# Performance work log

Measured on AMD Instinct MI355X. Metric: run time of the kernel, lower is better.

## Reference

```python
import jax, jax.numpy as jnp
import numpy as np

D = 512          # d_model
S = D // 2       # d_state
NL = 6           # num_layers
EVERY = 4        # attention_every
WIN = 256        # window_size
H = 8            # num_heads
DH = D // H      # head_dim
EPS = 1e-5


def layer_norm(x, gamma, beta):
    mu = jnp.mean(x, axis=-1, keepdims=True)
    var = jnp.mean((x - mu) ** 2, axis=-1, keepdims=True)
    return (x - mu) * jax.lax.rsqrt(var + EPS) * gamma + beta


def mamba_layer(seq, state, conv_w, Wx, Wh, Wout, A):
    """Lightweight Mamba-style update returning a (B, D) state summary.

    causal depthwise conv (k=3) -> SiLU -> project to d_state -> diagonal
    linear SSM scan (computed in closed form since the decay is constant)
    -> read out final state back to d_model.
    """
    B, L, _ = seq.shape
    xp = jnp.pad(seq, ((0, 0), (2, 0), (0, 0)))  # causal pad, kernel 3
    x = conv_w[0] * xp[:, :L] + conv_w[1] * xp[:, 1:L + 1] + conv_w[2] * xp[:, 2:L + 2]
    x = jax.nn.silu(x)
    u = jnp.einsum('bld,ds->bls', x, Wx)          # (B, L, S)
    a = jax.nn.sigmoid(A)                          # (S,) decay in (0,1)
    powers = (L - 1) - jnp.arange(L, dtype=jnp.float32)  # (L,)
    w = a[None, :] ** powers[:, None]              # (L, S)
    h0 = state @ Wh                                # (B, S)
    hT = (a ** L) * h0 + jnp.einsum('bls,ls->bs', u, w)
    return hT @ Wout                               # (B, D)


def local_attention(seq, Wqkv, bqkv, Wo, bo):
    B, L, _ = seq.shape
    qkv = seq @ Wqkv.T + bqkv                      # (B, L, 3D)
    q, k, v = jnp.split(qkv, 3, axis=-1)
    q = q.reshape(B, L, H, DH).transpose(0, 2, 1, 3)
    k = k.reshape(B, L, H, DH).transpose(0, 2, 1, 3)
    v = v.reshape(B, L, H, DH).transpose(0, 2, 1, 3)
    idx = jnp.arange(L)
    band = jnp.abs(idx[:, None] - idx[None, :]) <= WIN
    mask = jnp.where(band, 0.0, -jnp.inf).astype(seq.dtype)  # (L, L)
    scores = jnp.einsum('bhqd,bhkd->bhqk', q, k) / np.sqrt(DH) + mask
    attn = jax.nn.softmax(scores, axis=-1)
    out = jnp.einsum('bhqk,bhkd->bhqd', attn, v)
    out = out.transpose(0, 2, 1, 3).reshape(B, L, D)
    return out @ Wo.T + bo


def setup_inputs() -> dict:
    key = jax.random.key(0)
    ks = jax.random.split(key, 12)
    B, L = 4, 2048
    sc = 0.02
    return {
        'context': jax.random.normal(ks[0], (B, L, D), jnp.float32),
        'conv_w': jax.random.normal(ks[1], (NL, 3, D), jnp.float32) * sc,
        'Wx': jax.random.normal(ks[2], (NL, D, S), jnp.float32) * sc,
        'Wh': jax.random.normal(ks[3], (NL, D, S), jnp.float32) * sc,
        'Wout': jax.random.normal(ks[4], (NL, S, D), jnp.float32) * sc,
        'A': jax.random.normal(ks[5], (NL, S), jnp.float32),
        'gamma_m': jnp.ones((D,), jnp.float32),
        'beta_m': jnp.zeros((D,), jnp.float32),
        'gamma_a': jnp.ones((D,), jnp.float32),
        'beta_a': jnp.zeros((D,), jnp.float32),
        'Wqkv': jax.random.normal(ks[6], (3 * D, D), jnp.float32) * sc,
        'bqkv': jnp.zeros((3 * D,), jnp.float32),
        'Wo': jax.random.normal(ks[7], (D, D), jnp.float32) * sc,
        'bo': jnp.zeros((D,), jnp.float32),
    }


def reference(context, conv_w, Wx, Wh, Wout, A, gamma_m, beta_m, gamma_a, beta_a, Wqkv, bqkv, Wo, bo):
    B = context.shape[0]
    seq = context
    state = jnp.zeros((B, D), context.dtype)  # initial_state=None
    for i in range(NL):
        state = mamba_layer(seq, state, conv_w[i], Wx[i], Wh[i], Wout[i], A[i])
        seq = layer_norm(seq + state[:, None, :], gamma_m, beta_m)
        if (i + 1) % EVERY == 0:
            attn_out = local_attention(seq, Wqkv, bqkv, Wo, bo)
            seq = layer_norm(seq + attn_out, gamma_a, beta_a)
    return seq
```

## Files before the change

### kernel.cpp

```cpp
#include <hip/hip_runtime.h>

#define B_ 4
#define L_ 2048
#define D_ 512
#define S_ 256
#define H_ 8
#define DH_ 64
#define WIN_ 256
#define EPS_ 1e-5f
#define LOG2E_ 1.4426950408889634f
#define UWIN_ 768
#define UCHUNKS_ 6

using f32x4 = __attribute__((ext_vector_type(4))) float;
using s16x8 = __attribute__((ext_vector_type(8))) short;

__device__ __forceinline__ unsigned short f2b(float f) {
  unsigned int u = __builtin_bit_cast(unsigned int, f);
  u += 0x7FFFu + ((u >> 16) & 1u);
  return (unsigned short)(u >> 16);
}
__device__ __forceinline__ float b2f(unsigned short u) {
  return __builtin_bit_cast(float, (unsigned int)u << 16);
}

__device__ __forceinline__ float silu(float y) { return y / (1.f + expf(-y)); }

__device__ __forceinline__ void gll16(const void* g, void* l) {
  __builtin_amdgcn_global_load_lds((const __attribute__((address_space(1))) void*)g,
                                   (__attribute__((address_space(3))) void*)l, 16, 0, 0);
}

__global__ __launch_bounds__(256) void k_f2b(const float* __restrict__ in,
                                             unsigned short* __restrict__ out, int n4) {
  int i = blockIdx.x * 256 + threadIdx.x;
  if (i >= n4) return;
  float4 v = reinterpret_cast<const float4*>(in)[i];
  ushort4 o;
  o.x = f2b(v.x); o.y = f2b(v.y); o.z = f2b(v.z); o.w = f2b(v.w);
  reinterpret_cast<ushort4*>(out)[i] = o;
}

__global__ void k_twx(const float* __restrict__ wx, unsigned short* __restrict__ wxt) {
  __shared__ float tile[32][33];
  int lyr = blockIdx.z;
  int d0 = blockIdx.x * 32, s0 = blockIdx.y * 32;
  const float* src = wx + (size_t)lyr * D_ * S_;
  unsigned short* dst = wxt + (size_t)lyr * S_ * D_;
  for (int r = threadIdx.y; r < 32; r += 8)
    tile[r][threadIdx.x] = src[(size_t)(d0 + r) * S_ + s0 + threadIdx.x];
  __syncthreads();
  for (int r = threadIdx.y; r < 32; r += 8)
    dst[(size_t)(s0 + r) * D_ + d0 + threadIdx.x] = f2b(tile[threadIdx.x][r]);
}

__global__ __launch_bounds__(128) void k_conv_silu(const float* __restrict__ seq,
                                                   const float* __restrict__ cw,
                                                   unsigned short* __restrict__ x) {
  int bl = blockIdx.x;
  int l = bl & (L_ - 1);
  int t = threadIdx.x;
  const float4* s4 = reinterpret_cast<const float4*>(seq);
  const float4* c4 = reinterpret_cast<const float4*>(cw);
  size_t row = (size_t)bl * 128;
  float4 c0 = c4[t], c1 = c4[128 + t], c2 = c4[256 + t];
  float4 z = make_float4(0.f, 0.f, 0.f, 0.f);
  float4 s0 = (l >= 2) ? s4[row - 256 + t] : z;
  float4 s1 = (l >= 1) ? s4[row - 128 + t] : z;
  float4 s2 = s4[row + t];
  float y0 = c0.x * s0.x + c1.x * s1.x + c2.x * s2.x;
  float y1 = c0.y * s0.y + c1.y * s1.y + c2.y * s2.y;
  float y2 = c0.z * s0.z + c1.z * s1.z + c2.z * s2.z;
  float y3 = c0.w * s0.w + c1.w * s1.w + c2.w * s2.w;
  ushort4 o;
  o.x = f2b(silu(y0)); o.y = f2b(silu(y1)); o.z = f2b(silu(y2)); o.w = f2b(silu(y3));
  reinterpret_cast<ushort4*>(x)[row + t] = o;
}

__global__ __launch_bounds__(64) void k_lnconv(const void* __restrict__ seqIn, int in_bf16,
                                               const float* __restrict__ add, int addfull,
                                               const float* __restrict__ gamma,
                                               const float* __restrict__ beta,
                                               unsigned short* __restrict__ outBf,
                                               float* __restrict__ outF32,
                                               unsigned short* __restrict__ xbf,
                                               const float* __restrict__ cw) {
  int t = threadIdx.x;
  int r0 = blockIdx.x * 8;
  int b = r0 >> 11, l0 = r0 & (L_ - 1);
  bool hasconv = (cw != nullptr);
  const float4* in4 = reinterpret_cast<const float4*>(seqIn);
  const s16x8* inb = reinterpret_cast<const s16x8*>(seqIn);
  const float4* ad4 = reinterpret_cast<const float4*>(add);
  float4 g0 = reinterpret_cast<const float4*>(gamma)[2 * t];
  float4 g1 = reinterpret_cast<const float4*>(gamma)[2 * t + 1];
  float4 be0 = reinterpret_cast<const float4*>(beta)[2 * t];
  float4 be1 = reinterpret_cast<const float4*>(beta)[2 * t + 1];
  float4 av0, av1;
  if (!addfull) { av0 = ad4[b * 128 + 2 * t]; av1 = ad4[b * 128 + 2 * t + 1]; }
  float4 c0a, c0b, c1a, c1b, c2a, c2b;
  if (hasconv) {
    const float4* c4 = reinterpret_cast<const float4*>(cw);
    c0a = c4[2 * t]; c0b = c4[2 * t + 1];
    c1a = c4[128 + 2 * t]; c1b = c4[128 + 2 * t + 1];
    c2a = c4[256 + 2 * t]; c2b = c4[256 + 2 * t + 1];
  }
  float4 z = make_float4(0.f, 0.f, 0.f, 0.f);
  float4 m2a = z, m2b = z, m1a = z, m1b = z;
  int nrows = hasconv ? 10 : 8;
  int lstart = hasconv ? l0 - 2 : l0;
  for (int j = 0; j < nrows; ++j) {
    int l = lstart + j;
    float4 oa = z, ob = z;
    if (l >= 0) {
      size_t r4 = ((size_t)(b * L_ + l)) * 128;
      float4 v0, v1;
      if (in_bf16) {
        s16x8 v8 = inb[((size_t)(b * L_ + l)) * 64 + t];
        v0.x = b2f((unsigned short)v8[0]); v0.y = b2f((unsigned short)v8[1]);
        v0.z = b2f((unsigned short)v8[2]); v0.w = b2f((unsigned short)v8[3]);
        v1.x = b2f((unsigned short)v8[4]); v1.y = b2f((unsigned short)v8[5]);
        v1.z = b2f((unsigned short)v8[6]); v1.w = b2f((unsigned short)v8[7]);
      } else {
        v0 = in4[r4 + 2 * t]; v1 = in4[r4 + 2 * t + 1];
      }
      float4 a0, a1;
      if (addfull) { a0 = ad4[r4 + 2 * t]; a1 = ad4[r4 + 2 * t + 1]; }
      else { a0 = av0; a1 = av1; }
      v0.x += a0.x; v0.y += a0.y; v0.z += a0.z; v0.w += a0.w;
      v1.x += a1.x; v1.y += a1.y; v1.z += a1.z; v1.w += a1.w;
      float sx = v0.x + v0.y + v0.z + v0.w + v1.x + v1.y + v1.z + v1.w;
      float sq = v0.x * v0.x + v0.y * v0.y + v0.z * v0.z + v0.w * v0.w +
                 v1.x * v1.x + v1.y * v1.y + v1.z * v1.z + v1.w * v1.w;
#pragma unroll
      for (int off = 1; off < 64; off <<= 1) {
        sx += __shfl_xor(sx, off);
        sq += __shfl_xor(sq, off);
      }
      float mu = sx * (1.f / D_);
      float var = sq * (1.f / D_) - mu * mu;
      float rstd = rsqrtf(var + EPS_);
      oa.x = (v0.x - mu) * rstd * g0.x + be0.x;
      oa.y = (v0.y - mu) * rstd * g0.y + be0.y;
      oa.z = (v0.z - mu) * rstd * g0.z + be0.z;
      oa.w = (v0.w - mu) * rstd * g0.w + be0.w;
      ob.x = (v1.x - mu) * rstd * g1.x + be1.x;
      ob.y = (v1.y - mu) * rstd * g1.y + be1.y;
      ob.z = (v1.z - mu) * rstd * g1.z + be1.z;
      ob.w = (v1.w - mu) * rstd * g1.w + be1.w;
      if (l >= l0) {
        if (outBf) {
          s16x8 sb;
          sb[0] = (short)f2b(oa.x); sb[1] = (short)f2b(oa.y);
          sb[2] = (short)f2b(oa.z); sb[3] = (short)f2b(oa.w);
          sb[4] = (short)f2b(ob.x); sb[5] = (short)f2b(ob.y);
          sb[6] = (short)f2b(ob.z); sb[7] = (short)f2b(ob.w);
          *reinterpret_cast<s16x8*>(outBf + ((size_t)(b * L_ + l)) * 512 + t * 8) = sb;
        }
        if (outF32) {
          float4* o4 = reinterpret_cast<float4*>(outF32);
          o4[r4 + 2 * t] = oa;
          o4[r4 + 2 * t + 1] = ob;
        }
      }
    }
    if (hasconv && j >= 2) {
      float y0 = c0a.x * m2a.x + c1a.x * m1a.x + c2a.x * oa.x;
      float y1 = c0a.y * m2a.y + c1a.y * m1a.y + c2a.y * oa.y;
      float y2 = c0a.z * m2a.z + c1a.z * m1a.z + c2a.z * oa.z;
      float y3 = c0a.w * m2a.w + c1a.w * m1a.w + c2a.w * oa.w;
      float y4 = c0b.x * m2b.x + c1b.x * m1b.x + c2b.x * ob.x;
      float y5 = c0b.y * m2b.y + c1b.y * m1b.y + c2b.y * ob.y;
      float y6 = c0b.z * m2b.z + c1b.z * m1b.z + c2b.z * ob.z;
      float y7 = c0b.w * m2b.w + c1b.w * m1b.w + c2b.w * ob.w;
      s16x8 xo;
      xo[0] = (short)f2b(silu(y0)); xo[1] = (short)f2b(silu(y1));
      xo[2] = (short)f2b(silu(y2)); xo[3] = (short)f2b(silu(y3));
      xo[4] = (short)f2b(silu(y4)); xo[5] = (short)f2b(silu(y5));
      xo[6] = (short)f2b(silu(y6)); xo[7] = (short)f2b(silu(y7));
      *reinterpret_cast<s16x8*>(xbf + ((size_t)(b * L_ + l)) * 512 + t * 8) = xo;
    }
    m2a = m1a; m2b = m1b; m1a = oa; m1b = ob;
  }
}

__device__ __forceinline__ void g128_core(const unsigned short* __restrict__ A,
                                          const unsigned short* __restrict__ Bt,
                                          int K, int m0, int n0, int k_lo, int k_hi,
                                          unsigned short* As, unsigned short* Bs,
                                          f32x4 (&acc)[4][4]) {
  int t = threadIdx.x;
  int lane = t & 63;
  int g = lane >> 4, mr = lane & 15;
  int wid = t >> 6, wr = wid >> 1, wc = wid & 1;
#pragma unroll
  for (int i = 0; i < 4; ++i)
#pragma unroll
    for (int j = 0; j < 4; ++j) { f32x4 z = {0.f, 0.f, 0.f, 0.f}; acc[i][j] = z; }
  int r0 = t >> 2, p = (t & 3) * 8;
  const unsigned short* ag0 = A + (size_t)(m0 + r0) * K + p;
  const unsigned short* ag1 = ag0 + (size_t)64 * K;
  const unsigned short* bg0 = Bt + (size_t)(n0 + r0) * K + p;
  const unsigned short* bg1 = bg0 + (size_t)64 * K;
  int woff = wid * 512;
  gll16(ag0 + k_lo, As + woff);
  gll16(ag1 + k_lo, As + 2048 + woff);
  gll16(bg0 + k_lo, Bs + woff);
  gll16(bg1 + k_lo, Bs + 2048 + woff);
  int nsteps = (k_hi - k_lo) >> 5;
  int cur = 0;
  for (int s = 0; s < nsteps; ++s) {
    int k0 = k_lo + (s << 5);
    if (s + 1 < nsteps) {
      int nb = (cur ^ 1) * 4096;
      gll16(ag0 + k0 + 32, As + nb + woff);
      gll16(ag1 + k0 + 32, As + nb + 2048 + woff);
      gll16(bg0 + k0 + 32, Bs + nb + woff);
      gll16(bg1 + k0 + 32, Bs + nb + 2048 + woff);
      asm volatile("s_waitcnt vmcnt(4)" ::: "memory");
    } else {
      asm volatile("s_waitcnt vmcnt(0)" ::: "memory");
    }
    __builtin_amdgcn_sched_barrier(0);
    __builtin_amdgcn_s_barrier();
    __builtin_amdgcn_sched_barrier(0);
    const unsigned short* Ar = As + cur * 4096;
    const unsigned short* Br = Bs + cur * 4096;
    s16x8 af[4], bf[4];
#pragma unroll
    for (int fm = 0; fm < 4; ++fm)
      af[fm] = *reinterpret_cast<const s16x8*>(Ar + (size_t)(wr * 64 + fm * 16 + mr) * 32 + g * 8);
#pragma unroll
    for (int fn = 0; fn < 4; ++fn)
      bf[fn] = *reinterpret_cast<const s16x8*>(Br + (size_t)(wc * 64 + fn * 16 + mr) * 32 + g * 8);
#pragma unroll
    for (int fm = 0; fm < 4; ++fm)
#pragma unroll
      for (int fn = 0; fn < 4; ++fn)
        acc[fm][fn] = __builtin_amdgcn_mfma_f32_16x16x32_bf16(af[fm], bf[fn], acc[fm][fn], 0, 0, 0);
    __builtin_amdgcn_sched_barrier(0);
    __builtin_amdgcn_s_barrier();
    cur ^= 1;
  }
}

__device__ __forceinline__ int xcd_lb(int bid, int nwg) {
  return (bid & 7) * (nwg >> 3) + (bid >> 3);
}

__global__ __launch_bounds__(256) void k_g128(const unsigned short* __restrict__ A,
                                              const unsigned short* __restrict__ Bt,
                                              float* __restrict__ C,
                                              const float* __restrict__ bias,
                                              int N, int K, int ntn) {
  __shared__ __align__(16) unsigned short As[8192], Bs[8192];
  int lb = xcd_lb(blockIdx.x, gridDim.x);
  int m0 = (lb / ntn) * 128, n0 = (lb % ntn) * 128;
  f32x4 acc[4][4];
  g128_core(A, Bt, K, m0, n0, 0, K, As, Bs, acc);
  int t = threadIdx.x, lane = t & 63, g = lane >> 4, mr = lane & 15;
  int wid = t >> 6, wr = wid >> 1, wc = wid & 1;
#pragma unroll
  for (int fm = 0; fm < 4; ++fm)
#pragma unroll
    for (int fn = 0; fn < 4; ++fn) {
      int row = m0 + wr * 64 + fm * 16 + g * 4;
      int col = n0 + wc * 64 + fn * 16 + mr;
      float badd = bias ? bias[col] : 0.f;
#pragma unroll
      for (int q = 0; q < 4; ++q)
        C[(size_t)(row + q) * N + col] = acc[fm][fn][q] + badd;
    }
}

__global__ __launch_bounds__(256) void k_g128_qkv(const unsigned short* __restrict__ A,
                                                  const unsigned short* __restrict__ Bt,
                                                  const float* __restrict__ bias,
                                                  unsigned short* __restrict__ Qbf,
                                                  unsigned short* __restrict__ Kbf,
                                                  unsigned short* __restrict__ VbfT) {
  __shared__ __align__(16) unsigned short sm[16384];
  int lb = xcd_lb(blockIdx.x, gridDim.x);
  int m0 = (lb / 12) * 128, n0 = (lb % 12) * 128;
  f32x4 acc[4][4];
  g128_core(A, Bt, 512, m0, n0, 0, 512, sm, sm + 8192, acc);
  int t = threadIdx.x, lane = t & 63, g = lane >> 4, mr = lane & 15;
  int wid = t >> 6, wr = wid >> 1, wc = wid & 1;
  int b = m0 >> 11, l0 = m0 & (L_ - 1);
  if (n0 < 1024) {
#pragma unroll
    for (int fm = 0; fm < 4; ++fm)
#pragma unroll
      for (int fn = 0; fn < 4; ++fn) {
        int row0 = m0 + wr * 64 + fm * 16 + g * 4;
        int col = n0 + wc * 64 + fn * 16 + mr;
        int sec = col >> 9;
        int hh = (col >> 6) & 7;
        int dh = col & 63;
        float badd = bias[col];
        float scale = (sec == 0) ? 0.125f : 1.f;
        unsigned short* dstbase = (sec == 0) ? Qbf : Kbf;
#pragma unroll
        for (int q = 0; q < 4; ++q) {
          int row = row0 + q;
          int bb = row >> 11, l = row & (L_ - 1);
          dstbase[(((size_t)(bb * H_ + hh)) * L_ + l) * 64 + dh] =
              f2b((acc[fm][fn][q] + badd) * scale);
        }
      }
  } else {
#pragma unroll
    for (int chalf = 0; chalf < 2; ++chalf) {
      __syncthreads();
      if (wc == chalf) {
#pragma unroll
        for (int fm = 0; fm < 4; ++fm)
#pragma unroll
          for (int fn = 0; fn < 4; ++fn) {
            int col = n0 + wc * 64 + fn * 16 + mr;
            float badd = bias[col];
            int col_local = fn * 16 + mr;
            int row_local = wr * 64 + fm * 16 + g * 4;
            ushort4 pk;
            pk.x = f2b(acc[fm][fn][0] + badd);
            pk.y = f2b(acc[fm][fn][1] + badd);
            pk.z = f2b(acc[fm][fn][2] + badd);
            pk.w = f2b(acc[fm][fn][3] + badd);
            *reinterpret_cast<ushort4*>(&sm[col_local * 136 + row_local]) = pk;
          }
      }
      __syncthreads();
      int c = t >> 2, lp = (t & 3) * 32;
      int h = ((n0 - 1024) >> 6) + chalf;
      unsigned short* dst = VbfT + (((size_t)(b * H_ + h)) * 64 + c) * L_ + l0 + lp;
#pragma unroll
      for (int u = 0; u < 4; ++u)
        *reinterpret_cast<s16x8*>(dst + u * 8) =
            *reinterpret_cast<const s16x8*>(&sm[c * 136 + lp + u * 8]);
    }
  }
}

__global__ __launch_bounds__(256) void k_g128_u(const unsigned short* __restrict__ A,
                                                const unsigned short* __restrict__ Bt,
                                                const float* __restrict__ Ap,
                                                float* __restrict__ part3) {
  __shared__ __align__(16) unsigned short As[8192], Bs[8192];
  int lb = xcd_lb(blockIdx.x, gridDim.x);
  int mt = lb >> 3;
  int rr = lb & 7;
  int nt = rr >> 2, kz = rr & 3;
  int b = mt / UCHUNKS_, cc = mt % UCHUNKS_;
  int m0 = b * L_ + (L_ - UWIN_) + cc * 128;
  int n0 = nt * 128;
  f32x4 acc[4][4];
  g128_core(A, Bt, 512, m0, n0, kz * 128, kz * 128 + 128, As, Bs, acc);
  int t = threadIdx.x, lane = t & 63, g = lane >> 4, mr = lane & 15;
  int wid = t >> 6, wr = wid >> 1, wc = wid & 1;
  float wsum[4];
#pragma unroll
  for (int fn = 0; fn < 4; ++fn) {
    int col = n0 + wc * 64 + fn * 16 + mr;
    float a = 1.f / (1.f + expf(-Ap[col]));
    float la2 = log2f(a);
    float s = 0.f;
#pragma unroll
    for (int fm = 0; fm < 4; ++fm) {
      int rbase = (m0 + wr * 64 + fm * 16 + g * 4) & (L_ - 1);
#pragma unroll
      for (int q = 0; q < 4; ++q) {
        float e = (float)(2047 - (rbase + q));
        s += acc[fm][fn][q] * exp2f(e * la2);
      }
    }
    s += __shfl_xor(s, 16);
    s += __shfl_xor(s, 32);
    wsum[fn] = s;
  }
  float* red = (float*)As;
  __syncthreads();
  if (wr == 0 && g == 0) {
#pragma unroll
    for (int fn = 0; fn < 4; ++fn) red[(wc * 4 + fn) * 16 + mr] = wsum[fn];
  }
  __syncthreads();
  if (wr == 1 && g == 0) {
#pragma unroll
    for (int fn = 0; fn < 4; ++fn) {
      int col = n0 + wc * 64 + fn * 16 + mr;
      part3[(((size_t)(b * UCHUNKS_ + cc)) * 4 + kz) * 256 + col] =
          wsum[fn] + red[(wc * 4 + fn) * 16 + mr];
    }
  }
}

__global__ __launch_bounds__(256) void k_tail(const float* __restrict__ part3,
                                              const float* __restrict__ Wout,
                                              float* __restrict__ state) {
  int bz = blockIdx.x;
  int b = bz >> 4, dl = (bz & 15) * 32;
  int t = threadIdx.x;
  __shared__ float hTs[256];
  __shared__ float red[8][33];
  float acc = 0.f;
#pragma unroll
  for (int c = 0; c < UCHUNKS_ * 4; ++c)
    acc += part3[((size_t)b * UCHUNKS_ * 4 + c) * 256 + t];
  hTs[t] = acc;
  __syncthreads();
  int dx = t & 31, sy = t >> 5;
  float p = 0.f;
  for (int j = 0; j < 32; ++j) {
    int s = sy * 32 + j;
    p += hTs[s] * Wout[(size_t)s * 512 + dl + dx];
  }
  red[sy][dx] = p;
  __syncthreads();
  if (t < 32) {
    float a = 0.f;
#pragma unroll
    for (int k = 0; k < 8; ++k) a += red[k][t];
    state[b * 512 + dl + t] = a;
  }
}

__global__ __launch_bounds__(256) void k_fattn(const unsigned short* __restrict__ Qbf,
                                               const unsigned short* __restrict__ Kbf,
                                               const unsigned short* __restrict__ VbfT,
                                               unsigned short* __restrict__ attnbf) {
  __shared__ __align__(16) unsigned short Ks[64][72];
  __shared__ __align__(16) unsigned short Vt[64][72];
  __shared__ __align__(16) unsigned short Ps[4][16][72];
  int b = blockIdx.z, h = blockIdx.y, q0 = blockIdx.x * 64;
  int t = threadIdx.x;
  int lane = t & 63, wid = t >> 6;
  int g = lane >> 4, mr = lane & 15;
  const unsigned short* Qp = Qbf + ((size_t)(b * H_ + h)) * L_ * 64;
  const unsigned short* Kp = Kbf + ((size_t)(b * H_ + h)) * L_ * 64;
  const unsigned short* VpT = VbfT + ((size_t)(b * H_ + h)) * 64 * L_;
  int qbase = q0 + wid * 16;
  s16x8 qf0 = *reinterpret_cast<const s16x8*>(Qp + (size_t)(qbase + mr) * 64 + g * 8);
  s16x8 qf1 = *reinterpret_cast<const s16x8*>(Qp + (size_t)(qbase + mr) * 64 + 32 + g * 8);
  f32x4 oacc[4];
#pragma unroll
  for (int fn = 0; fn < 4; ++fn) { f32x4 zz = {0.f, 0.f, 0.f, 0.f}; oacc[fn] = zz; }
  float lsum[4] = {0.f, 0.f, 0.f, 0.f};
  int kstart = q0 - WIN_; if (kstart < 0) kstart = 0;
  int kend = q0 + 64 + WIN_; if (kend > L_) kend = L_;

  for (int kt = kstart; kt < kend; kt += 64) {
    __syncthreads();
#pragma unroll
    for (int it = 0; it < 2; ++it) {
      int chunk = t + it * 256;
      int row = chunk >> 3, c8 = (chunk & 7) * 8;
      *reinterpret_cast<s16x8*>(&Ks[row][c8]) =
          *reinterpret_cast<const s16x8*>(Kp + (size_t)(kt + row) * 64 + c8);
      *reinterpret_cast<s16x8*>(&Vt[row][c8]) =
          *reinterpret_cast<const s16x8*>(VpT + (size_t)row * L_ + kt + c8);
    }
    __syncthreads();
    f32x4 sacc[4];
#pragma unroll
    for (int n = 0; n < 4; ++n) {
      f32x4 zz = {0.f, 0.f, 0.f, 0.f};
      sacc[n] = zz;
      s16x8 kf0 = *reinterpret_cast<const s16x8*>(&Ks[n * 16 + mr][g * 8]);
      s16x8 kf1 = *reinterpret_cast<const s16x8*>(&Ks[n * 16 + mr][32 + g * 8]);
      sacc[n] = __builtin_amdgcn_mfma_f32_16x16x32_bf16(qf0, kf0, sacc[n], 0, 0, 0);
      sacc[n] = __builtin_amdgcn_mfma_f32_16x16x32_bf16(qf1, kf1, sacc[n], 0, 0, 0);
    }
    bool needmask = (kt - q0 > 192) || (q0 - kt > 192);
#pragma unroll
    for (int reg = 0; reg < 4; ++reg) {
      int q_abs = qbase + g * 4 + reg;
#pragma unroll
      for (int n = 0; n < 4; ++n) {
        float pv = exp2f(sacc[n][reg] * LOG2E_);
        if (needmask) {
          int key = kt + n * 16 + mr;
          int dd = key - q_abs; dd = dd < 0 ? -dd : dd;
          if (dd > WIN_) pv = 0.f;
        }
        lsum[reg] += pv;
        Ps[wid][g * 4 + reg][n * 16 + mr] = f2b(pv);
      }
    }
    s16x8 pa0 = *reinterpret_cast<const s16x8*>(&Ps[wid][mr][g * 8]);
    s16x8 pa1 = *reinterpret_cast<const s16x8*>(&Ps[wid][mr][32 + g * 8]);
#pragma unroll
    for (int fn = 0; fn < 4; ++fn) {
      s16x8 vf0 = *reinterpret_cast<const s16x8*>(&Vt[fn * 16 + mr][g * 8]);
      s16x8 vf1 = *reinterpret_cast<const s16x8*>(&Vt[fn * 16 + mr][32 + g * 8]);
      oacc[fn] = __builtin_amdgcn_mfma_f32_16x16x32_bf16(pa0, vf0, oacc[fn], 0, 0, 0);
      oacc[fn] = __builtin_amdgcn_mfma_f32_16x16x32_bf16(pa1, vf1, oacc[fn], 0, 0, 0);
    }
  }
#pragma unroll
  for (int reg = 0; reg < 4; ++reg) {
    float ls = lsum[reg];
#pragma unroll
    for (int off = 1; off < 16; off <<= 1) ls += __shfl_xor(ls, off);
    float inv = 1.f / ls;
    int q_abs = qbase + g * 4 + reg;
    unsigned short* dst = attnbf + ((size_t)(b * L_ + q_abs)) * 512 + h * 64;
#pragma unroll
    for (int fn = 0; fn < 4; ++fn)
      dst[fn * 16 + mr] = f2b(oacc[fn][reg] * inv);
  }
}

extern "C" void kernel_launch(void* const* d_in, const int* in_sizes, int n_in,
                              void* d_out, int out_size, void* d_ws, size_t ws_size,
                              hipStream_t stream) {
  const float* context = (const float*)d_in[0];
  const float* conv_w  = (const float*)d_in[1];
  const float* Wx      = (const float*)d_in[2];
  const float* Wout    = (const float*)d_in[4];
  const float* Aparm   = (const float*)d_in[5];
  const float* gamma_m = (const float*)d_in[6];
  const float* beta_m  = (const float*)d_in[7];
  const float* gamma_a = (const float*)d_in[8];
  const float* beta_a  = (const float*)d_in[9];
  const float* Wqkv    = (const float*)d_in[10];
  const float* bqkv    = (const float*)d_in[11];
  const float* Wo      = (const float*)d_in[12];
  const float* bo      = (const float*)d_in[13];
  float* outF = (float*)d_out;
  float* ws = (float*)d_ws;

  float* proj = ws;
  unsigned short* Qbf    = (unsigned short*)(ws);
  unsigned short* Kbf    = (unsigned short*)(ws + 2097152);
  unsigned short* seqAb  = (unsigned short*)(ws + 4194304);
  unsigned short* seqBb  = (unsigned short*)(ws + 6291456);
  unsigned short* VbfT   = (unsigned short*)(ws + 8388608);
  unsigned short* xbf    = (unsigned short*)(ws + 10485760);
  unsigned short* attnbf = (unsigned short*)(ws + 12582912);
  unsigned short* wqkvbf = (unsigned short*)(ws + 14680064);
  unsigned short* wobf   = (unsigned short*)(ws + 15073280);
  unsigned short* wxtbf  = (unsigned short*)(ws + 15204352);
  float* state = ws + 15597568;
  float* part3 = state + 2048;

  k_f2b<<<768, 256, 0, stream>>>(Wqkv, wqkvbf, 196608);
  k_f2b<<<256, 256, 0, stream>>>(Wo, wobf, 65536);
  k_twx<<<dim3(16, 8, 6), dim3(32, 8), 0, stream>>>(Wx, wxtbf);

  k_conv_silu<<<B_ * L_, 128, 0, stream>>>(context, conv_w, xbf);

  for (int i = 0; i < 6; ++i) {
    k_g128_u<<<B_ * UCHUNKS_ * 8, 256, 0, stream>>>(
        xbf, wxtbf + (size_t)i * S_ * D_, Aparm + (size_t)i * S_, part3);
    k_tail<<<64, 256, 0, stream>>>(part3, Wout + (size_t)i * S_ * D_, state);
    const float* cwn = conv_w + (size_t)(i + 1) * 3 * D_;
    switch (i) {
      case 0:
        k_lnconv<<<1024, 64, 0, stream>>>(context, 0, state, 0, gamma_m, beta_m,
                                          seqAb, nullptr, xbf, cwn);
        break;
      case 1:
        k_lnconv<<<1024, 64, 0, stream>>>(seqAb, 1, state, 0, gamma_m, beta_m,
                                          seqBb, nullptr, xbf, cwn);
        break;
      case 2:
        k_lnconv<<<1024, 64, 0, stream>>>(seqBb, 1, state, 0, gamma_m, beta_m,
                                          seqAb, nullptr, xbf, cwn);
        break;
      case 3:
        k_lnconv<<<1024, 64, 0, stream>>>(seqAb, 1, state, 0, gamma_m, beta_m,
                                          seqAb, nullptr, nullptr, nullptr);
        k_g128_qkv<<<768, 256, 0, stream>>>(seqAb, wqkvbf, bqkv, Qbf, Kbf, VbfT);
        k_fattn<<<dim3(32, 8, 4), 256, 0, stream>>>(Qbf, Kbf, VbfT, attnbf);
        k_g128<<<256, 256, 0, stream>>>(attnbf, wobf, proj, bo, 512, 512, 4);
        k_lnconv<<<1024, 64, 0, stream>>>(seqAb, 1, proj, 1, gamma_a, beta_a,
                                          seqBb, nullptr, xbf, cwn);
        break;
      case 4:
        k_lnconv<<<1024, 64, 0, stream>>>(seqBb, 1, state, 0, gamma_m, beta_m,
                                          seqAb, nullptr, xbf, cwn);
        break;
      case 5:
        k_lnconv<<<1024, 64, 0, stream>>>(seqAb, 1, state, 0, gamma_m, beta_m,
                                          nullptr, outF, nullptr, nullptr);
        break;
    }
  }
}
```

Baseline: 257.8 us.

## Fuse SSM tail into u-GEMM via last-block atomic counter; merge weight casts

Removes the separate k_tail launch per layer. The last GEMM block to finish for each batch, found through an atomic counter, now reduces the partial sums and does the Wout readout itself. The two fp32-to-bf16 weight conversion kernels are merged into one launch. The cost is that the readout now runs on only 4 blocks, one per batch, each doing a serial 256-step loop instead of spreading over 64 blocks. It also adds a memset and threadfence overhead.

After: 395.6 us. 53.4% more time.

```diff
diff --git a/kernel.cpp b/kernel.cpp
--- a/kernel.cpp
+++ b/kernel.cpp
@@ -31,14 +31,20 @@
                                    (__attribute__((address_space(3))) void*)l, 16, 0, 0);
 }
 
-__global__ __launch_bounds__(256) void k_f2b(const float* __restrict__ in,
-                                             unsigned short* __restrict__ out, int n4) {
+__global__ __launch_bounds__(256) void k_f2b2(const float* __restrict__ inA,
+                                              unsigned short* __restrict__ outA, int na4,
+                                              const float* __restrict__ inB,
+                                              unsigned short* __restrict__ outB, int nb4) {
   int i = blockIdx.x * 256 + threadIdx.x;
-  if (i >= n4) return;
-  float4 v = reinterpret_cast<const float4*>(in)[i];
+  const float* src;
+  unsigned short* dst;
+  int j;
+  if (i < na4) { src = inA; dst = outA; j = i; }
+  else { j = i - na4; if (j >= nb4) return; src = inB; dst = outB; }
+  float4 v = reinterpret_cast<const float4*>(src)[j];
   ushort4 o;
   o.x = f2b(v.x); o.y = f2b(v.y); o.z = f2b(v.z); o.w = f2b(v.w);
-  reinterpret_cast<ushort4*>(out)[i] = o;
+  reinterpret_cast<ushort4*>(dst)[j] = o;
 }
 
 __global__ void k_twx(const float* __restrict__ wx, unsigned short* __restrict__ wxt) {
@@ -341,11 +347,15 @@
   }
 }
 
-__global__ __launch_bounds__(256) void k_g128_u(const unsigned short* __restrict__ A,
-                                                const unsigned short* __restrict__ Bt,
-                                                const float* __restrict__ Ap,
-                                                float* __restrict__ part3) {
+__global__ __launch_bounds__(256) void k_g128_ut(const unsigned short* __restrict__ A,
+                                                 const unsigned short* __restrict__ Bt,
+                                                 const float* __restrict__ Ap,
+                                                 float* __restrict__ part3,
+                                                 const float* __restrict__ Wout,
+                                                 float* __restrict__ state,
+                                                 int* __restrict__ cnt) {
   __shared__ __align__(16) unsigned short As[8192], Bs[8192];
+  __shared__ int isLast;
   int lb = xcd_lb(blockIdx.x, gridDim.x);
   int mt = lb >> 3;
   int rr = lb & 7;
@@ -392,35 +402,31 @@
           wsum[fn] + red[(wc * 4 + fn) * 16 + mr];
     }
   }
-}
-
-__global__ __launch_bounds__(256) void k_tail(const float* __restrict__ part3,
-                                              const float* __restrict__ Wout,
-                                              float* __restrict__ state) {
-  int bz = blockIdx.x;
-  int b = bz >> 4, dl = (bz & 15) * 32;
-  int t = threadIdx.x;
-  __shared__ float hTs[256];
-  __shared__ float red[8][33];
-  float acc = 0.f;
-#pragma unroll
-  for (int c = 0; c < UCHUNKS_ * 4; ++c)
-    acc += part3[((size_t)b * UCHUNKS_ * 4 + c) * 256 + t];
-  hTs[t] = acc;
+  __threadfence();
   __syncthreads();
-  int dx = t & 31, sy = t >> 5;
-  float p = 0.f;
-  for (int j = 0; j < 32; ++j) {
-    int s = sy * 32 + j;
-    p += hTs[s] * Wout[(size_t)s * 512 + dl + dx];
-  }
-  red[sy][dx] = p;
+  if (t == 0) {
+    int v = atomicAdd(&cnt[b], 1);
+    isLast = (v == 47) ? 1 : 0;
+  }
   __syncthreads();
-  if (t < 32) {
-    float a = 0.f;
-#pragma unroll
-    for (int k = 0; k < 8; ++k) a += red[k][t];
-    state[b * 512 + dl + t] = a;
+  if (isLast) {
+    __threadfence();
+    float h = 0.f;
+#pragma unroll
+    for (int c = 0; c < UCHUNKS_ * 4; ++c)
+      h += __hip_atomic_load(&part3[((size_t)b * UCHUNKS_ * 4 + c) * 256 + t],
+                             __ATOMIC_RELAXED, __HIP_MEMORY_SCOPE_AGENT);
+    float* hTs = (float*)As;
+    hTs[t] = h;
+    __syncthreads();
+    float s0 = 0.f, s1 = 0.f;
+    for (int s = 0; s < 256; ++s) {
+      float hv = hTs[s];
+      s0 += hv * Wout[(size_t)s * 512 + t];
+      s1 += hv * Wout[(size_t)s * 512 + t + 256];
+    }
+    state[b * 512 + t] = s0;
+    state[b * 512 + t + 256] = s1;
   }
 }
 
@@ -542,17 +548,18 @@
   unsigned short* wxtbf  = (unsigned short*)(ws + 15204352);
   float* state = ws + 15597568;
   float* part3 = state + 2048;
-
-  k_f2b<<<768, 256, 0, stream>>>(Wqkv, wqkvbf, 196608);
-  k_f2b<<<256, 256, 0, stream>>>(Wo, wobf, 65536);
+  int*   cnt   = (int*)(part3 + 24576);
+
+  hipMemsetAsync(cnt, 0, 24 * sizeof(int), stream);
+  k_f2b2<<<1024, 256, 0, stream>>>(Wqkv, wqkvbf, 196608, Wo, wobf, 65536);
   k_twx<<<dim3(16, 8, 6), dim3(32, 8), 0, stream>>>(Wx, wxtbf);
 
   k_conv_silu<<<B_ * L_, 128, 0, stream>>>(context, conv_w, xbf);
 
   for (int i = 0; i < 6; ++i) {
-    k_g128_u<<<B_ * UCHUNKS_ * 8, 256, 0, stream>>>(
-        xbf, wxtbf + (size_t)i * S_ * D_, Aparm + (size_t)i * S_, part3);
-    k_tail<<<64, 256, 0, stream>>>(part3, Wout + (size_t)i * S_ * D_, state);
+    k_g128_ut<<<B_ * UCHUNKS_ * 8, 256, 0, stream>>>(
+        xbf, wxtbf + (size_t)i * S_ * D_, Aparm + (size_t)i * S_, part3,
+        Wout + (size_t)i * S_ * D_, state, cnt + i * 4);
     const float* cwn = conv_w + (size_t)(i + 1) * 3 * D_;
     switch (i) {
       case 0:
```
